# Kernel optimization log

Hardware: AMD Instinct MI355X
Metric: run time of the kernel (lower is better)

Reference implementation:

```python
import jax, jax.numpy as jnp
from jax import lax
import numpy as np

K = 1024      # kernel_size
S = 256       # stride
CUT = 513     # kernel_size//2 + 1
TC = 2 * CUT  # transform_channels = 1026
CH = 8        # combine_hidden
B = 32
TIME = 262144


def setup_inputs() -> dict:
    key = jax.random.key(0)
    ks = jax.random.split(key, 12)
    x = jax.random.normal(ks[0], (B, 1, TIME), dtype=jnp.float32)
    conv1_w = jax.random.normal(ks[1], (TC, 1, K), dtype=jnp.float32) * 0.02
    in_gamma = 1.0 + 0.1 * jax.random.normal(ks[2], (TC,), dtype=jnp.float32)
    comb1_w = jax.random.normal(ks[3], (CH, 2), dtype=jnp.float32) * 0.5
    comb1_b = jax.random.normal(ks[4], (CH,), dtype=jnp.float32) * 0.1
    comb2_w = jax.random.normal(ks[5], (1, CH), dtype=jnp.float32) * 0.5
    comb2_b = jax.random.normal(ks[6], (1,), dtype=jnp.float32) * 0.1
    lin_w = jax.random.normal(ks[7], (CUT, CUT), dtype=jnp.float32) * 0.04
    lin_b = jax.random.normal(ks[8], (CUT,), dtype=jnp.float32) * 0.02
    fc_gamma = 1.0 + 0.1 * jax.random.normal(ks[9], (CUT,), dtype=jnp.float32)
    convT_w = jax.random.normal(ks[10], (TC, 2, K), dtype=jnp.float32) * 0.02  # torch ConvTranspose1d (Cin, Cout, K)
    return {"x": x, "conv1_w": conv1_w, "in_gamma": in_gamma,
            "comb1_w": comb1_w, "comb1_b": comb1_b,
            "comb2_w": comb2_w, "comb2_b": comb2_b,
            "lin_w": lin_w, "lin_b": lin_b, "fc_gamma": fc_gamma,
            "convT_w": convT_w}


def reference(x, conv1_w, in_gamma, comb1_w, comb1_b, comb2_w, comb2_b,
              lin_w, lin_b, fc_gamma, convT_w):
    time = x.shape[2]
    # conv1: Conv1d(1, TC, K, stride=S, padding=K), no bias
    t = lax.conv_general_dilated(x, conv1_w, window_strides=(S,),
                                 padding=[(K, K)],
                                 dimension_numbers=("NCH", "OIH", "NCH"))
    # ConvScaler1d (per-channel scale) + tanh activation
    t = jnp.tanh(t * in_gamma[None, :, None])  # (B, TC, F)
    real_x, imag_x = t[:, :CUT, :], t[:, CUT:, :]
    spec = jnp.stack([real_x, imag_x], axis=1)  # (B, 2, CUT, F)
    # combine1/combine2: 1x1 Conv2d + relu
    h = jax.nn.relu(jnp.einsum("bcxf,oc->boxf", spec, comb1_w)
                    + comb1_b[None, :, None, None])
    h = jax.nn.relu(jnp.einsum("bcxf,oc->boxf", h, comb2_w)
                    + comb2_b[None, :, None, None])[:, 0]  # (B, CUT, F)
    # FC over frequency axis per (batch, frame)
    hh = h.transpose(0, 2, 1)  # (B, F, CUT)
    hh = (hh @ lin_w.T + lin_b) * fc_gamma  # BitwiseLinear + Scaler
    mask = (jnp.tanh(hh) + 1.0) * 0.5       # output_transform -> [0,1]
    mask = mask.transpose(0, 2, 1)          # (B, CUT, F)
    mask = jnp.concatenate([mask, mask], axis=1)  # (B, TC, F)
    t = t * mask
    # conv1_transpose: ConvTranspose1d(TC, 2, K, stride=S), no bias
    wt = jnp.flip(convT_w.transpose(1, 0, 2), axis=2)  # (2, TC, K) flipped
    y = lax.conv_general_dilated(t, wt, window_strides=(1,),
                                 padding=[(K - 1, K - 1)],
                                 lhs_dilation=(S,),
                                 dimension_numbers=("NCH", "OIH", "NCH"))
    y = y[:, :, K:time + K]  # (B, 2, time)
    return jax.nn.softmax(y, axis=1)
```

## Files before the change

kernel.cpp:

```cpp
#include <hip/hip_runtime.h>
#include <cstddef>
#include <cstdint>

#define TIME_N 262144
#define BATCH  32
#define KW     1024
#define ST     256
#define CUTN   513
#define TCN    1026
#define FN     1029
#define FPAD   1152
#define CPAD   1152
#define XLEN   (FPAD * ST + KW)
#define XBLK   (XLEN / 256)

#define MROWS  (BATCH * FN)
#define MP     33024
#define KPH    544
#define NPH    640
#define TBP    1032
#define FLATB  (FN * TBP)
#define KPC    4128

#define PB_XPAD  (XBLK * BATCH)
#define PB_WBF   (PB_XPAD + CPAD)
#define PB_WLIN  (PB_WBF + NPH)
#define PB_TOTAL (PB_WLIN + KPC)

typedef __bf16 bf16x8 __attribute__((ext_vector_type(8)));
typedef float floatx4 __attribute__((ext_vector_type(4)));

__device__ __forceinline__ unsigned short f2bf(float f) {
    union { float f; unsigned u; } v; v.f = f;
    unsigned r = (v.u + 0x7fffu + ((v.u >> 16) & 1u)) >> 16;
    return (unsigned short)r;
}
__device__ __forceinline__ float bf2f(unsigned short s) {
    union { unsigned u; float f; } v; v.u = ((unsigned)s) << 16;
    return v.f;
}
__device__ __forceinline__ int permch(int n) {
    return (n & 1) ? (CUTN + (n >> 1)) : (n >> 1);
}

__device__ __forceinline__ void load_lds16(const void* g, void* l) {
    __builtin_amdgcn_global_load_lds(
        (const __attribute__((address_space(1))) void*)g,
        (__attribute__((address_space(3))) void*)l, 16, 0, 0);
}

__global__ __launch_bounds__(256) void k_prep(
    const float* __restrict__ x, const float* __restrict__ c1w,
    const float* __restrict__ lw, const float* __restrict__ wct,
    unsigned short* __restrict__ xb, unsigned short* __restrict__ wbf,
    unsigned short* __restrict__ wlb, unsigned short* __restrict__ wdb)
{
    const int bid = blockIdx.x;
    if (bid < PB_XPAD) {
        const int b = bid / XBLK;
        const int p = (bid - b * XBLK) * 256 + threadIdx.x;
        const int g = p - KW;
        float v = (g >= 0 && g < TIME_N) ? x[(size_t)b * TIME_N + g] : 0.0f;
        xb[(size_t)b * XLEN + p] = f2bf(v);
    } else if (bid < PB_WBF) {
        const int n = bid - PB_XPAD;
        const int ch = (n < TCN) ? permch(n) : 0;
        for (int k = threadIdx.x; k < KW; k += 256) {
            float v = (n < TCN) ? c1w[(size_t)ch * KW + k] : 0.0f;
            wbf[(size_t)n * KW + k] = f2bf(v);
        }
    } else if (bid < PB_WLIN) {
        const int n = bid - PB_WBF;
        for (int k = threadIdx.x; k < KPH; k += 256) {
            float v = (n < CUTN && k < CUTN) ? lw[(size_t)n * CUTN + k] : 0.0f;
            wlb[(size_t)n * KPH + k] = f2bf(v);
        }
    } else {
        const int k = bid - PB_WLIN;
        const int r = threadIdx.x;
        const int j = k / TBP;
        const int n = k - j * TBP;
        float v = 0.0f;
        if (n < TCN) {
            const int ch = permch(n);
            const int widx = (3 - j) * 256 + r;
            v = wct[(size_t)(2 * ch) * KW + widx] -
                wct[(size_t)(2 * ch + 1) * KW + widx];
        }
        wdb[(size_t)r * KPC + k] = f2bf(v);
    }
}

__global__ __launch_bounds__(256) void k_conv1m(
    const unsigned short* __restrict__ xb, const unsigned short* __restrict__ wb,
    const float* __restrict__ gamma,
    const float* __restrict__ c1w, const float* __restrict__ c1b,
    const float* __restrict__ c2w, const float* __restrict__ c2b,
    unsigned short* __restrict__ tb2, unsigned short* __restrict__ h)
{
    __shared__ __align__(16) unsigned short As[128 * 32];
    __shared__ __align__(16) unsigned short Bs[128 * 32];

    const int b = blockIdx.x, fb = blockIdx.y, cb = blockIdx.z;
    const int f0 = fb * 128, c0 = cb * 128;
    const int tid = threadIdx.x;

    const int s0 = tid, s1 = tid + 256;
    const int ar0 = s0 >> 2, aq0 = s0 & 3;
    const int ar1 = s1 >> 2, aq1 = s1 & 3;
    const unsigned short* xrow = xb + (size_t)b * XLEN;
    const unsigned short* ga0 = xrow + (size_t)(f0 + ar0) * ST + aq0 * 8;
    const unsigned short* ga1 = xrow + (size_t)(f0 + ar1) * ST + aq1 * 8;
    const unsigned short* gb0 = wb + (size_t)(c0 + ar0) * KW + aq0 * 8;
    const unsigned short* gb1 = wb + (size_t)(c0 + ar1) * KW + aq1 * 8;
    unsigned short* la0 = &As[s0 * 8];
    unsigned short* la1 = &As[s1 * 8];
    unsigned short* lb0 = &Bs[s0 * 8];
    unsigned short* lb1 = &Bs[s1 * 8];

    const int wave = tid >> 6, lane = tid & 63;
    const int lm = lane & 15, lq = lane >> 4;
    const int mw = (wave & 1) * 64, nw = (wave >> 1) * 64;
    const unsigned short* Ap = &As[(mw + lm) * 32 + lq * 8];
    const unsigned short* Bp = &Bs[(nw + lm) * 32 + lq * 8];

    floatx4 acc[4][4];
#pragma unroll
    for (int i = 0; i < 4; ++i)
#pragma unroll
        for (int j = 0; j < 4; ++j) acc[i][j] = (floatx4)0.0f;

    for (int ks = 0; ks < KW / 32; ++ks) {
        load_lds16(ga0, la0);
        load_lds16(ga1, la1);
        load_lds16(gb0, lb0);
        load_lds16(gb1, lb1);
        ga0 += 32; ga1 += 32; gb0 += 32; gb1 += 32;
        __syncthreads();

        bf16x8 afr[4], bfr[4];
#pragma unroll
        for (int mt = 0; mt < 4; ++mt) afr[mt] = *(const bf16x8*)(Ap + mt * 16 * 32);
#pragma unroll
        for (int nt = 0; nt < 4; ++nt) bfr[nt] = *(const bf16x8*)(Bp + nt * 16 * 32);
#pragma unroll
        for (int mt = 0; mt < 4; ++mt)
#pragma unroll
            for (int nt = 0; nt < 4; ++nt)
                acc[mt][nt] = __builtin_amdgcn_mfma_f32_16x16x32_bf16(
                    afr[mt], bfr[nt], acc[mt][nt], 0, 0, 0);
        __syncthreads();
    }

    float w1[16], b1[8], w2[8];
#pragma unroll
    for (int o = 0; o < 8; ++o) {
        w1[2 * o]     = c1w[2 * o];
        w1[2 * o + 1] = c1w[2 * o + 1];
        b1[o] = c1b[o];
        w2[o] = c2w[o];
    }
    const float b2v = c2b[0];

    unsigned short* tbb = tb2 + (size_t)b * FLATB;
    const bool evenlane = ((lane & 1) == 0);
#pragma unroll
    for (int nt = 0; nt < 4; ++nt) {
        const int n = c0 + nw + nt * 16 + lm;
        const bool valid_c = (n < TCN);
        const float gv = valid_c ? gamma[permch(n)] : 0.0f;
        const int nbase = n & ~1;
        const int ybase = n >> 1;
        const bool store_c = (nbase < TBP);
#pragma unroll
        for (int mt = 0; mt < 4; ++mt) {
#pragma unroll
            for (int rp = 0; rp < 2; ++rp) {
                const int ra = rp * 2;
                const int fa = f0 + mw + mt * 16 + lq * 4 + ra;
                const float ua = acc[mt][nt][ra] * gv;
                const float ub = acc[mt][nt][ra + 1] * gv;
                const float ta  = 2.0f / (1.0f + __expf(-2.0f * ua)) - 1.0f;
                const float tbv = 2.0f / (1.0f + __expf(-2.0f * ub)) - 1.0f;
                const float sa = __shfl_xor(ta, 1);
                const float sb = __shfl_xor(tbv, 1);
                const int  fme = evenlane ? fa : (fa + 1);
                const float re = evenlane ? ta : sb;
                const float im = evenlane ? sa : tbv;
                if (fme < FN) {
                    if (store_c) {
                        const unsigned pr = (unsigned)f2bf(re) |
                                            ((unsigned)f2bf(im) << 16);
                        *(unsigned*)&tbb[(size_t)fme * TBP + nbase] = pr;
                    }
                    if (valid_c) {
                        float a2 = b2v;
#pragma unroll
                        for (int o = 0; o < 8; ++o) {
                            const float a1 = fmaxf(
                                re * w1[2 * o] + im * w1[2 * o + 1] + b1[o], 0.0f);
                            a2 += a1 * w2[o];
                        }
                        h[((size_t)b * FN + fme) * KPH + ybase] =
                            f2bf(fmaxf(a2, 0.0f));
                    }
                }
            }
        }
    }
}

__global__ __launch_bounds__(256) void k_maskm(
    const unsigned short* __restrict__ h, const unsigned short* __restrict__ wlb,
    const float* __restrict__ linb, const float* __restrict__ fcg,
    unsigned* __restrict__ tbu)
{
    __shared__ __align__(16) unsigned short As[128 * 32];
    __shared__ __align__(16) unsigned short Bs[128 * 32];

    const int m0 = blockIdx.x * 128, n0 = blockIdx.y * 128;
    const int tid = threadIdx.x;

    const int s0 = tid, s1 = tid + 256;
    const int ar0 = s0 >> 2, aq0 = s0 & 3;
    const int ar1 = s1 >> 2, aq1 = s1 & 3;
    const unsigned short* ga0 = h + (size_t)(m0 + ar0) * KPH + aq0 * 8;
    const unsigned short* ga1 = h + (size_t)(m0 + ar1) * KPH + aq1 * 8;
    const unsigned short* gb0 = wlb + (size_t)(n0 + ar0) * KPH + aq0 * 8;
    const unsigned short* gb1 = wlb + (size_t)(n0 + ar1) * KPH + aq1 * 8;
    unsigned short* la0 = &As[s0 * 8];
    unsigned short* la1 = &As[s1 * 8];
    unsigned short* lb0 = &Bs[s0 * 8];
    unsigned short* lb1 = &Bs[s1 * 8];

    const int wave = tid >> 6, lane = tid & 63;
    const int lm = lane & 15, lq = lane >> 4;
    const int mw = (wave & 1) * 64, nw = (wave >> 1) * 64;
    const unsigned short* Ap = &As[(mw + lm) * 32 + lq * 8];
    const unsigned short* Bp = &Bs[(nw + lm) * 32 + lq * 8];

    floatx4 acc[4][4];
#pragma unroll
    for (int i = 0; i < 4; ++i)
#pragma unroll
        for (int j = 0; j < 4; ++j) acc[i][j] = (floatx4)0.0f;

    for (int ks = 0; ks < KPH / 32; ++ks) {
        load_lds16(ga0, la0);
        load_lds16(ga1, la1);
        load_lds16(gb0, lb0);
        load_lds16(gb1, lb1);
        ga0 += 32; ga1 += 32; gb0 += 32; gb1 += 32;
        __syncthreads();

        bf16x8 afr[4], bfr[4];
#pragma unroll
        for (int mt = 0; mt < 4; ++mt) afr[mt] = *(const bf16x8*)(Ap + mt * 16 * 32);
#pragma unroll
        for (int nt = 0; nt < 4; ++nt) bfr[nt] = *(const bf16x8*)(Bp + nt * 16 * 32);
#pragma unroll
        for (int mt = 0; mt < 4; ++mt)
#pragma unroll
            for (int nt = 0; nt < 4; ++nt)
                acc[mt][nt] = __builtin_amdgcn_mfma_f32_16x16x32_bf16(
                    afr[mt], bfr[nt], acc[mt][nt], 0, 0, 0);
        __syncthreads();
    }

#pragma unroll
    for (int nt = 0; nt < 4; ++nt) {
        const int y = n0 + nw + nt * 16 + lm;
        if (y < CUTN) {
            const float lb = linb[y];
            const float gv = fcg[y];
#pragma unroll
            for (int mt = 0; mt < 4; ++mt) {
#pragma unroll
                for (int r = 0; r < 4; ++r) {
                    const int m = m0 + mw + mt * 16 + lq * 4 + r;
                    if (m < MROWS) {
                        const float v = (acc[mt][nt][r] + lb) * gv;
                        const float msk = 1.0f / (1.0f + __expf(-2.0f * v));
                        unsigned* p = tbu + (size_t)m * (TBP / 2) + y;
                        const unsigned u = *p;
                        const float re = bf2f((unsigned short)(u & 0xffffu)) * msk;
                        const float im = bf2f((unsigned short)(u >> 16)) * msk;
                        *p = (unsigned)f2bf(re) | ((unsigned)f2bf(im) << 16);
                    }
                }
            }
        }
    }
}

__global__ __launch_bounds__(256) void k_convtm(
    const unsigned short* __restrict__ tb2, const unsigned short* __restrict__ wdb,
    float* __restrict__ out)
{
    __shared__ __align__(16) unsigned short As[128 * 32];
    __shared__ __align__(16) unsigned short Bs[128 * 32];

    const int m0 = blockIdx.x * 128, n0 = blockIdx.y * 128;
    const int b   = m0 >> 10;
    const int ml0 = m0 & 1023;
    const int tid = threadIdx.x;

    const int s0 = tid, s1 = tid + 256;
    const int ar0 = s0 >> 2, aq0 = s0 & 3;
    const int ar1 = s1 >> 2, aq1 = s1 & 3;
    const unsigned short* tbb = tb2 + (size_t)b * FLATB;
    const unsigned short* ga0 = tbb + (size_t)(ml0 + ar0 + 1) * TBP + aq0 * 8;
    const unsigned short* ga1 = tbb + (size_t)(ml0 + ar1 + 1) * TBP + aq1 * 8;
    const unsigned short* gb0 = wdb + (size_t)(n0 + ar0) * KPC + aq0 * 8;
    const unsigned short* gb1 = wdb + (size_t)(n0 + ar1) * KPC + aq1 * 8;
    unsigned short* la0 = &As[s0 * 8];
    unsigned short* la1 = &As[s1 * 8];
    unsigned short* lb0 = &Bs[s0 * 8];
    unsigned short* lb1 = &Bs[s1 * 8];

    const int wave = tid >> 6, lane = tid & 63;
    const int lm = lane & 15, lq = lane >> 4;
    const int mw = (wave & 1) * 64, nw = (wave >> 1) * 64;
    const unsigned short* Ap = &As[(mw + lm) * 32 + lq * 8];
    const unsigned short* Bp = &Bs[(nw + lm) * 32 + lq * 8];

    floatx4 acc[4][4];
#pragma unroll
    for (int i = 0; i < 4; ++i)
#pragma unroll
        for (int j = 0; j < 4; ++j) acc[i][j] = (floatx4)0.0f;

    for (int ks = 0; ks < KPC / 32; ++ks) {
        load_lds16(ga0, la0);
        load_lds16(ga1, la1);
        load_lds16(gb0, lb0);
        load_lds16(gb1, lb1);
        ga0 += 32; ga1 += 32; gb0 += 32; gb1 += 32;
        __syncthreads();

        bf16x8 afr[4], bfr[4];
#pragma unroll
        for (int mt = 0; mt < 4; ++mt) afr[mt] = *(const bf16x8*)(Ap + mt * 16 * 32);
#pragma unroll
        for (int nt = 0; nt < 4; ++nt) bfr[nt] = *(const bf16x8*)(Bp + nt * 16 * 32);
#pragma unroll
        for (int mt = 0; mt < 4; ++mt)
#pragma unroll
            for (int nt = 0; nt < 4; ++nt)
                acc[mt][nt] = __builtin_amdgcn_mfma_f32_16x16x32_bf16(
                    afr[mt], bfr[nt], acc[mt][nt], 0, 0, 0);
        __syncthreads();
    }

    float* ob = out + (size_t)b * 2 * TIME_N;
#pragma unroll
    for (int nt = 0; nt < 4; ++nt) {
        const int n = n0 + nw + nt * 16 + lm;
#pragma unroll
        for (int mt = 0; mt < 4; ++mt) {
#pragma unroll
            for (int r = 0; r < 4; ++r) {
                const int m = ml0 + mw + mt * 16 + lq * 4 + r;
                const float d = acc[mt][nt][r];
                const float p0 = 1.0f / (1.0f + __expf(-d));
                const int tau = m * 256 + n;
                ob[tau]          = p0;
                ob[TIME_N + tau] = 1.0f - p0;
            }
        }
    }
}

extern "C" void kernel_launch(void* const* d_in, const int* in_sizes, int n_in,
                              void* d_out, int out_size, void* d_ws, size_t ws_size,
                              hipStream_t stream)
{
    const float* x    = (const float*)d_in[0];
    const float* c1w  = (const float*)d_in[1];
    const float* ing  = (const float*)d_in[2];
    const float* cb1w = (const float*)d_in[3];
    const float* cb1b = (const float*)d_in[4];
    const float* cb2w = (const float*)d_in[5];
    const float* cb2b = (const float*)d_in[6];
    const float* linw = (const float*)d_in[7];
    const float* linb = (const float*)d_in[8];
    const float* fcg  = (const float*)d_in[9];
    const float* ctw  = (const float*)d_in[10];
    float* out = (float*)d_out;

    unsigned short* tb2 = (unsigned short*)d_ws;
    unsigned short* h   = tb2 + (size_t)BATCH * FLATB;
    unsigned short* wlb = h + (size_t)MP * KPH;
    unsigned short* xb  = wlb + (size_t)NPH * KPH;
    unsigned short* wbf = xb + (size_t)BATCH * XLEN;
    unsigned short* wdb = wbf + (size_t)CPAD * KW;

    hipLaunchKernelGGL(k_prep, dim3(PB_TOTAL), dim3(256), 0, stream,
                       x, c1w, linw, ctw, xb, wbf, wlb, wdb);
    hipLaunchKernelGGL(k_conv1m, dim3(BATCH, 9, 9), dim3(256), 0, stream,
                       xb, wbf, ing, cb1w, cb1b, cb2w, cb2b, tb2, h);
    hipLaunchKernelGGL(k_maskm, dim3(MP / 128, NPH / 128), dim3(256), 0, stream,
                       h, wlb, linb, fcg, (unsigned*)tb2);
    hipLaunchKernelGGL(k_convtm, dim3(256, 2), dim3(256), 0, stream,
                       tb2, wdb, out);
}
```

Measured before the change: 512.0 us.

## Retile conv1 GEMM to 256x256x64 with double-buffered swizzled LDS

Rewrites the conv1 im2col GEMM kernel to use 256x256 tiles with BK=64 and 512 threads. Batch and frame are flattened into one M dimension. LDS is double-buffered in 64KB halves with an XOR swizzle, so the next tile loads while the MFMAs run, and s_setprio and barriers interleave fragment loads with compute. The goal is to cut per-tile global/LDS traffic and barrier stalls and raise MFMA utilisation. The cost is 128KB of dynamic LDS, high register pressure, and partial tiles in N (1026 of 1280 columns used), which wastes some work.

```diff
diff --git a/kernel.cpp b/kernel.cpp
--- a/kernel.cpp
+++ b/kernel.cpp
@@ -26,6 +26,14 @@
 #define PB_WBF   (PB_XPAD + CPAD)
 #define PB_WLIN  (PB_WBF + NPH)
 #define PB_TOTAL (PB_WLIN + KPC)
+
+#define C1_BM   256
+#define C1_BN   256
+#define C1_BK   64
+#define C1_NT   (KW / C1_BK)
+#define C1_MB   129
+#define C1_NB   5
+#define C1_BUF  65536
 
 typedef __bf16 bf16x8 __attribute__((ext_vector_type(8)));
 typedef float floatx4 __attribute__((ext_vector_type(4)));
@@ -91,118 +99,209 @@
     }
 }
 
-__global__ __launch_bounds__(256) void k_conv1m(
+__global__ __launch_bounds__(512, 2) void k_conv1m(
     const unsigned short* __restrict__ xb, const unsigned short* __restrict__ wb,
     const float* __restrict__ gamma,
     const float* __restrict__ c1w, const float* __restrict__ c1b,
     const float* __restrict__ c2w, const float* __restrict__ c2b,
     unsigned short* __restrict__ tb2, unsigned short* __restrict__ h)
 {
-    __shared__ __align__(16) unsigned short As[128 * 32];
-    __shared__ __align__(16) unsigned short Bs[128 * 32];
-
-    const int b = blockIdx.x, fb = blockIdx.y, cb = blockIdx.z;
-    const int f0 = fb * 128, c0 = cb * 128;
+    extern __shared__ char lds[];
+    const int m0 = blockIdx.x * C1_BM;
+    const int n0 = blockIdx.y * C1_BN;
     const int tid = threadIdx.x;
-
-    const int s0 = tid, s1 = tid + 256;
-    const int ar0 = s0 >> 2, aq0 = s0 & 3;
-    const int ar1 = s1 >> 2, aq1 = s1 & 3;
-    const unsigned short* xrow = xb + (size_t)b * XLEN;
-    const unsigned short* ga0 = xrow + (size_t)(f0 + ar0) * ST + aq0 * 8;
-    const unsigned short* ga1 = xrow + (size_t)(f0 + ar1) * ST + aq1 * 8;
-    const unsigned short* gb0 = wb + (size_t)(c0 + ar0) * KW + aq0 * 8;
-    const unsigned short* gb1 = wb + (size_t)(c0 + ar1) * KW + aq1 * 8;
-    unsigned short* la0 = &As[s0 * 8];
-    unsigned short* la1 = &As[s1 * 8];
-    unsigned short* lb0 = &Bs[s0 * 8];
-    unsigned short* lb1 = &Bs[s1 * 8];
-
-    const int wave = tid >> 6, lane = tid & 63;
+    const int wv = tid >> 6, lane = tid & 63;
     const int lm = lane & 15, lq = lane >> 4;
-    const int mw = (wave & 1) * 64, nw = (wave >> 1) * 64;
-    const unsigned short* Ap = &As[(mw + lm) * 32 + lq * 8];
-    const unsigned short* Bp = &Bs[(nw + lm) * 32 + lq * 8];
-
-    floatx4 acc[4][4];
-#pragma unroll
-    for (int i = 0; i < 4; ++i)
+    const int wr = wv >> 2, wc = wv & 3;
+
+    const unsigned short* src[8];
+    int ldsq[8];
+#pragma unroll
+    for (int i = 0; i < 8; ++i) {
+        const int c = wv * 8 + i;
+        const int q = c * 1024 + lane * 16;
+        ldsq[i] = q;
+        const int sec = q >> 14;
+        const int p = q & 16383;
+        const int row = p >> 7;
+        const int cb = (p & 127) ^ ((row & 7) << 4);
+        const int e = cb >> 1;
+        if (sec < 2) {
+            int m = m0 + sec * 128 + row;
+            if (m >= MROWS) m = 0;
+            const int b = m / FN;
+            const int f = m - b * FN;
+            src[i] = xb + (size_t)b * XLEN + (size_t)f * ST + e;
+        } else {
+            int n = n0 + (sec - 2) * 128 + row;
+            if (n > CPAD - 1) n = CPAD - 1;
+            src[i] = wb + (size_t)n * KW + e;
+        }
+    }
+
+    const int swz = (lm & 7) << 4;
+    int abo[2], bbo[2];
+#pragma unroll
+    for (int ks = 0; ks < 2; ++ks) {
+        abo[ks] = wr * 16384 + lm * 128 + ((ks * 64 + lq * 16) ^ swz);
+        bbo[ks] = 32768 + (wc >> 1) * 16384 + ((wc & 1) * 64 + lm) * 128
+                  + ((ks * 64 + lq * 16) ^ swz);
+    }
+
+    floatx4 acc[8][4];
+#pragma unroll
+    for (int i = 0; i < 8; ++i)
 #pragma unroll
         for (int j = 0; j < 4; ++j) acc[i][j] = (floatx4)0.0f;
 
-    for (int ks = 0; ks < KW / 32; ++ks) {
-        load_lds16(ga0, la0);
-        load_lds16(ga1, la1);
-        load_lds16(gb0, lb0);
-        load_lds16(gb1, lb1);
-        ga0 += 32; ga1 += 32; gb0 += 32; gb1 += 32;
+#pragma unroll
+    for (int i = 0; i < 8; ++i) {
+        load_lds16(src[i], lds + ldsq[i]);
+        src[i] += C1_BK;
+    }
+    __syncthreads();
+
+    for (int t = 0; t < C1_NT; ++t) {
+        char* cur = lds + (t & 1) * C1_BUF;
+        char* nxt = lds + ((t + 1) & 1) * C1_BUF;
+        bf16x8 af[4][2], bf[2][2];
+
+#pragma unroll
+        for (int mt = 0; mt < 4; ++mt)
+#pragma unroll
+            for (int ks = 0; ks < 2; ++ks)
+                af[mt][ks] = *(const bf16x8*)(cur + abo[ks] + mt * 2048);
+#pragma unroll
+        for (int nt = 0; nt < 2; ++nt)
+#pragma unroll
+            for (int ks = 0; ks < 2; ++ks)
+                bf[nt][ks] = *(const bf16x8*)(cur + bbo[ks] + nt * 2048);
+        if (t + 1 < C1_NT) {
+#pragma unroll
+            for (int i = 0; i < 8; ++i) {
+                load_lds16(src[i], nxt + ldsq[i]);
+                src[i] += C1_BK;
+            }
+        }
+        __builtin_amdgcn_s_barrier();
+        __builtin_amdgcn_s_setprio(1);
+#pragma unroll
+        for (int mt = 0; mt < 4; ++mt)
+#pragma unroll
+            for (int nt = 0; nt < 2; ++nt)
+#pragma unroll
+                for (int ks = 0; ks < 2; ++ks)
+                    acc[mt][nt] = __builtin_amdgcn_mfma_f32_16x16x32_bf16(
+                        af[mt][ks], bf[nt][ks], acc[mt][nt], 0, 0, 0);
+        __builtin_amdgcn_s_setprio(0);
+        __builtin_amdgcn_s_barrier();
+
+#pragma unroll
+        for (int nt = 0; nt < 2; ++nt)
+#pragma unroll
+            for (int ks = 0; ks < 2; ++ks)
+                bf[nt][ks] = *(const bf16x8*)(cur + bbo[ks] + (2 + nt) * 2048);
+        __builtin_amdgcn_s_barrier();
+        __builtin_amdgcn_s_setprio(1);
+#pragma unroll
+        for (int mt = 0; mt < 4; ++mt)
+#pragma unroll
+            for (int nt = 0; nt < 2; ++nt)
+#pragma unroll
+                for (int ks = 0; ks < 2; ++ks)
+                    acc[mt][2 + nt] = __builtin_amdgcn_mfma_f32_16x16x32_bf16(
+                        af[mt][ks], bf[nt][ks], acc[mt][2 + nt], 0, 0, 0);
+        __builtin_amdgcn_s_setprio(0);
+        __builtin_amdgcn_s_barrier();
+
+#pragma unroll
+        for (int mt = 0; mt < 4; ++mt)
+#pragma unroll
+            for (int ks = 0; ks < 2; ++ks)
+                af[mt][ks] = *(const bf16x8*)(cur + abo[ks] + (4 + mt) * 2048);
+        __builtin_amdgcn_s_barrier();
+        __builtin_amdgcn_s_setprio(1);
+#pragma unroll
+        for (int mt = 0; mt < 4; ++mt)
+#pragma unroll
+            for (int nt = 0; nt < 2; ++nt)
+#pragma unroll
+                for (int ks = 0; ks < 2; ++ks)
+                    acc[4 + mt][2 + nt] = __builtin_amdgcn_mfma_f32_16x16x32_bf16(
+                        af[mt][ks], bf[nt][ks], acc[4 + mt][2 + nt], 0, 0, 0);
+        __builtin_amdgcn_s_setprio(0);
+        __builtin_amdgcn_s_barrier();
+
+#pragma unroll
+        for (int nt = 0; nt < 2; ++nt)
+#pragma unroll
+            for (int ks = 0; ks < 2; ++ks)
+                bf[nt][ks] = *(const bf16x8*)(cur + bbo[ks] + nt * 2048);
+        __builtin_amdgcn_s_barrier();
+        __builtin_amdgcn_s_setprio(1);
+#pragma unroll
+        for (int mt = 0; mt < 4; ++mt)
+#pragma unroll
+            for (int nt = 0; nt < 2; ++nt)
+#pragma unroll
+                for (int ks = 0; ks < 2; ++ks)
+                    acc[4 + mt][nt] = __builtin_amdgcn_mfma_f32_16x16x32_bf16(
+                        af[mt][ks], bf[nt][ks], acc[4 + mt][nt], 0, 0, 0);
+        __builtin_amdgcn_s_setprio(0);
         __syncthreads();
-
-        bf16x8 afr[4], bfr[4];
-#pragma unroll
-        for (int mt = 0; mt < 4; ++mt) afr[mt] = *(const bf16x8*)(Ap + mt * 16 * 32);
-#pragma unroll
-        for (int nt = 0; nt < 4; ++nt) bfr[nt] = *(const bf16x8*)(Bp + nt * 16 * 32);
-#pragma unroll
-        for (int mt = 0; mt < 4; ++mt)
-#pragma unroll
-            for (int nt = 0; nt < 4; ++nt)
-                acc[mt][nt] = __builtin_amdgcn_mfma_f32_16x16x32_bf16(
-                    afr[mt], bfr[nt], acc[mt][nt], 0, 0, 0);
-        __syncthreads();
-    }
-
-    float w1[16], b1[8], w2[8];
+    }
+
+    float w1[16], b1v[8], w2[8];
 #pragma unroll
     for (int o = 0; o < 8; ++o) {
         w1[2 * o]     = c1w[2 * o];
         w1[2 * o + 1] = c1w[2 * o + 1];
-        b1[o] = c1b[o];
+        b1v[o] = c1b[o];
         w2[o] = c2w[o];
     }
     const float b2v = c2b[0];
-
-    unsigned short* tbb = tb2 + (size_t)b * FLATB;
     const bool evenlane = ((lane & 1) == 0);
-#pragma unroll
-    for (int nt = 0; nt < 4; ++nt) {
-        const int n = c0 + nw + nt * 16 + lm;
+
+#pragma unroll
+    for (int ni = 0; ni < 4; ++ni) {
+        const int n = n0 + wc * 64 + ni * 16 + lm;
         const bool valid_c = (n < TCN);
         const float gv = valid_c ? gamma[permch(n)] : 0.0f;
         const int nbase = n & ~1;
         const int ybase = n >> 1;
         const bool store_c = (nbase < TBP);
 #pragma unroll
-        for (int mt = 0; mt < 4; ++mt) {
+        for (int mi = 0; mi < 8; ++mi) {
 #pragma unroll
             for (int rp = 0; rp < 2; ++rp) {
                 const int ra = rp * 2;
-                const int fa = f0 + mw + mt * 16 + lq * 4 + ra;
-                const float ua = acc[mt][nt][ra] * gv;
-                const float ub = acc[mt][nt][ra + 1] * gv;
+                const int mrow = m0 + wr * 128 + mi * 16 + lq * 4 + ra;
+                const float ua = acc[mi][ni][ra] * gv;
+                const float ub = acc[mi][ni][ra + 1] * gv;
                 const float ta  = 2.0f / (1.0f + __expf(-2.0f * ua)) - 1.0f;
                 const float tbv = 2.0f / (1.0f + __expf(-2.0f * ub)) - 1.0f;
                 const float sa = __shfl_xor(ta, 1);
                 const float sb = __shfl_xor(tbv, 1);
-                const int  fme = evenlane ? fa : (fa + 1);
+                const int  fme = evenlane ? mrow : (mrow + 1);
                 const float re = evenlane ? ta : sb;
                 const float im = evenlane ? sa : tbv;
-                if (fme < FN) {
+                if (fme < MROWS) {
+                    const int b = fme / FN;
+                    const int f = fme - b * FN;
                     if (store_c) {
                         const unsigned pr = (unsigned)f2bf(re) |
                                             ((unsigned)f2bf(im) << 16);
-                        *(unsigned*)&tbb[(size_t)fme * TBP + nbase] = pr;
+                        *(unsigned*)&tb2[(size_t)b * FLATB + (size_t)f * TBP + nbase] = pr;
                     }
                     if (valid_c) {
                         float a2 = b2v;
 #pragma unroll
                         for (int o = 0; o < 8; ++o) {
                             const float a1 = fmaxf(
-                                re * w1[2 * o] + im * w1[2 * o + 1] + b1[o], 0.0f);
+                                re * w1[2 * o] + im * w1[2 * o + 1] + b1v[o], 0.0f);
                             a2 += a1 * w2[o];
                         }
-                        h[((size_t)b * FN + fme) * KPH + ybase] =
-                            f2bf(fmaxf(a2, 0.0f));
+                        h[(size_t)fme * KPH + ybase] = f2bf(fmaxf(a2, 0.0f));
                     }
                 }
             }
@@ -397,7 +496,7 @@
 
     hipLaunchKernelGGL(k_prep, dim3(PB_TOTAL), dim3(256), 0, stream,
                        x, c1w, linw, ctw, xb, wbf, wlb, wdb);
-    hipLaunchKernelGGL(k_conv1m, dim3(BATCH, 9, 9), dim3(256), 0, stream,
+    hipLaunchKernelGGL(k_conv1m, dim3(C1_MB, C1_NB), dim3(512), 2 * C1_BUF, stream,
                        xb, wbf, ing, cb1w, cb1b, cb2w, cb2b, tb2, h);
     hipLaunchKernelGGL(k_maskm, dim3(MP / 128, NPH / 128), dim3(256), 0, stream,
                        h, wlb, linb, fcg, (unsigned*)tb2);
```

Measured after the change: 629.4 us. 22.9% more time.

## Double GEMM K-tile to 64 and XOR-swizzle LDS layout in conv kernels

Applied to the files above, without the earlier changes.

Both MFMA GEMM kernels (conv1 and transposed conv) now stage 64-wide K slices per iteration instead of 32, which halves the number of barrier pairs per K loop. The LDS tiles use an XOR swizzle on 16-byte chunks keyed by row, so fragment reads avoid bank conflicts. TBP and KPC padding grow to multiples of 64 so the K loop divides evenly. In exchange, LDS per block doubles and register pressure rises with two fragments per tile, which could reduce occupancy.

```diff
diff --git a/kernel.cpp b/kernel.cpp
--- a/kernel.cpp
+++ b/kernel.cpp
@@ -18,9 +18,9 @@
 #define MP     33024
 #define KPH    544
 #define NPH    640
-#define TBP    1032
+#define TBP    1040
 #define FLATB  (FN * TBP)
-#define KPC    4128
+#define KPC    4160
 
 #define PB_XPAD  (XBLK * BATCH)
 #define PB_WBF   (PB_XPAD + CPAD)
@@ -98,31 +98,38 @@
     const float* __restrict__ c2w, const float* __restrict__ c2b,
     unsigned short* __restrict__ tb2, unsigned short* __restrict__ h)
 {
-    __shared__ __align__(16) unsigned short As[128 * 32];
-    __shared__ __align__(16) unsigned short Bs[128 * 32];
+    __shared__ __align__(16) unsigned short As[128 * 64];
+    __shared__ __align__(16) unsigned short Bs[128 * 64];
 
     const int b = blockIdx.x, fb = blockIdx.y, cb = blockIdx.z;
     const int f0 = fb * 128, c0 = cb * 128;
     const int tid = threadIdx.x;
 
-    const int s0 = tid, s1 = tid + 256;
-    const int ar0 = s0 >> 2, aq0 = s0 & 3;
-    const int ar1 = s1 >> 2, aq1 = s1 & 3;
     const unsigned short* xrow = xb + (size_t)b * XLEN;
-    const unsigned short* ga0 = xrow + (size_t)(f0 + ar0) * ST + aq0 * 8;
-    const unsigned short* ga1 = xrow + (size_t)(f0 + ar1) * ST + aq1 * 8;
-    const unsigned short* gb0 = wb + (size_t)(c0 + ar0) * KW + aq0 * 8;
-    const unsigned short* gb1 = wb + (size_t)(c0 + ar1) * KW + aq1 * 8;
-    unsigned short* la0 = &As[s0 * 8];
-    unsigned short* la1 = &As[s1 * 8];
-    unsigned short* lb0 = &Bs[s0 * 8];
-    unsigned short* lb1 = &Bs[s1 * 8];
+    const unsigned short* ga[4];
+    const unsigned short* gb[4];
+    int qa[4];
+#pragma unroll
+    for (int i = 0; i < 4; ++i) {
+        const int c = i * 256 + tid;
+        const int row = c >> 3;
+        const int colb = (c & 7) * 16;
+        const int es = (colb ^ ((row & 7) << 4)) >> 1;
+        qa[i] = c * 16;
+        ga[i] = xrow + (size_t)(f0 + row) * ST + es;
+        gb[i] = wb + (size_t)(c0 + row) * KW + es;
+    }
 
     const int wave = tid >> 6, lane = tid & 63;
     const int lm = lane & 15, lq = lane >> 4;
     const int mw = (wave & 1) * 64, nw = (wave >> 1) * 64;
-    const unsigned short* Ap = &As[(mw + lm) * 32 + lq * 8];
-    const unsigned short* Bp = &Bs[(nw + lm) * 32 + lq * 8];
+    const int swz = (lm & 7) << 4;
+    int abo[2], bbo[2];
+#pragma unroll
+    for (int ks = 0; ks < 2; ++ks) {
+        abo[ks] = (mw + lm) * 128 + ((ks * 64 + lq * 16) ^ swz);
+        bbo[ks] = (nw + lm) * 128 + ((ks * 64 + lq * 16) ^ swz);
+    }
 
     floatx4 acc[4][4];
 #pragma unroll
@@ -130,25 +137,37 @@
 #pragma unroll
         for (int j = 0; j < 4; ++j) acc[i][j] = (floatx4)0.0f;
 
-    for (int ks = 0; ks < KW / 32; ++ks) {
-        load_lds16(ga0, la0);
-        load_lds16(ga1, la1);
-        load_lds16(gb0, lb0);
-        load_lds16(gb1, lb1);
-        ga0 += 32; ga1 += 32; gb0 += 32; gb1 += 32;
-        __syncthreads();
-
-        bf16x8 afr[4], bfr[4];
-#pragma unroll
-        for (int mt = 0; mt < 4; ++mt) afr[mt] = *(const bf16x8*)(Ap + mt * 16 * 32);
-#pragma unroll
-        for (int nt = 0; nt < 4; ++nt) bfr[nt] = *(const bf16x8*)(Bp + nt * 16 * 32);
+    const char* Ab = (const char*)As;
+    const char* Bb = (const char*)Bs;
+
+    for (int t = 0; t < KW / 64; ++t) {
+#pragma unroll
+        for (int i = 0; i < 4; ++i) {
+            load_lds16(ga[i], (char*)As + qa[i]);
+            load_lds16(gb[i], (char*)Bs + qa[i]);
+            ga[i] += 64; gb[i] += 64;
+        }
+        __syncthreads();
+
+        bf16x8 afr[4][2], bfr[4][2];
 #pragma unroll
         for (int mt = 0; mt < 4; ++mt)
 #pragma unroll
+            for (int ks = 0; ks < 2; ++ks)
+                afr[mt][ks] = *(const bf16x8*)(Ab + abo[ks] + mt * 2048);
+#pragma unroll
+        for (int nt = 0; nt < 4; ++nt)
+#pragma unroll
+            for (int ks = 0; ks < 2; ++ks)
+                bfr[nt][ks] = *(const bf16x8*)(Bb + bbo[ks] + nt * 2048);
+#pragma unroll
+        for (int mt = 0; mt < 4; ++mt)
+#pragma unroll
             for (int nt = 0; nt < 4; ++nt)
-                acc[mt][nt] = __builtin_amdgcn_mfma_f32_16x16x32_bf16(
-                    afr[mt], bfr[nt], acc[mt][nt], 0, 0, 0);
+#pragma unroll
+                for (int ks = 0; ks < 2; ++ks)
+                    acc[mt][nt] = __builtin_amdgcn_mfma_f32_16x16x32_bf16(
+                        afr[mt][ks], bfr[nt][ks], acc[mt][nt], 0, 0, 0);
         __syncthreads();
     }
 
@@ -297,32 +316,39 @@
     const unsigned short* __restrict__ tb2, const unsigned short* __restrict__ wdb,
     float* __restrict__ out)
 {
-    __shared__ __align__(16) unsigned short As[128 * 32];
-    __shared__ __align__(16) unsigned short Bs[128 * 32];
+    __shared__ __align__(16) unsigned short As[128 * 64];
+    __shared__ __align__(16) unsigned short Bs[128 * 64];
 
     const int m0 = blockIdx.x * 128, n0 = blockIdx.y * 128;
     const int b   = m0 >> 10;
     const int ml0 = m0 & 1023;
     const int tid = threadIdx.x;
 
-    const int s0 = tid, s1 = tid + 256;
-    const int ar0 = s0 >> 2, aq0 = s0 & 3;
-    const int ar1 = s1 >> 2, aq1 = s1 & 3;
     const unsigned short* tbb = tb2 + (size_t)b * FLATB;
-    const unsigned short* ga0 = tbb + (size_t)(ml0 + ar0 + 1) * TBP + aq0 * 8;
-    const unsigned short* ga1 = tbb + (size_t)(ml0 + ar1 + 1) * TBP + aq1 * 8;
-    const unsigned short* gb0 = wdb + (size_t)(n0 + ar0) * KPC + aq0 * 8;
-    const unsigned short* gb1 = wdb + (size_t)(n0 + ar1) * KPC + aq1 * 8;
-    unsigned short* la0 = &As[s0 * 8];
-    unsigned short* la1 = &As[s1 * 8];
-    unsigned short* lb0 = &Bs[s0 * 8];
-    unsigned short* lb1 = &Bs[s1 * 8];
+    const unsigned short* ga[4];
+    const unsigned short* gb[4];
+    int qa[4];
+#pragma unroll
+    for (int i = 0; i < 4; ++i) {
+        const int c = i * 256 + tid;
+        const int row = c >> 3;
+        const int colb = (c & 7) * 16;
+        const int es = (colb ^ ((row & 7) << 4)) >> 1;
+        qa[i] = c * 16;
+        ga[i] = tbb + (size_t)(ml0 + row + 1) * TBP + es;
+        gb[i] = wdb + (size_t)(n0 + row) * KPC + es;
+    }
 
     const int wave = tid >> 6, lane = tid & 63;
     const int lm = lane & 15, lq = lane >> 4;
     const int mw = (wave & 1) * 64, nw = (wave >> 1) * 64;
-    const unsigned short* Ap = &As[(mw + lm) * 32 + lq * 8];
-    const unsigned short* Bp = &Bs[(nw + lm) * 32 + lq * 8];
+    const int swz = (lm & 7) << 4;
+    int abo[2], bbo[2];
+#pragma unroll
+    for (int ks = 0; ks < 2; ++ks) {
+        abo[ks] = (mw + lm) * 128 + ((ks * 64 + lq * 16) ^ swz);
+        bbo[ks] = (nw + lm) * 128 + ((ks * 64 + lq * 16) ^ swz);
+    }
 
     floatx4 acc[4][4];
 #pragma unroll
@@ -330,25 +356,37 @@
 #pragma unroll
         for (int j = 0; j < 4; ++j) acc[i][j] = (floatx4)0.0f;
 
-    for (int ks = 0; ks < KPC / 32; ++ks) {
-        load_lds16(ga0, la0);
-        load_lds16(ga1, la1);
-        load_lds16(gb0, lb0);
-        load_lds16(gb1, lb1);
-        ga0 += 32; ga1 += 32; gb0 += 32; gb1 += 32;
-        __syncthreads();
-
-        bf16x8 afr[4], bfr[4];
-#pragma unroll
-        for (int mt = 0; mt < 4; ++mt) afr[mt] = *(const bf16x8*)(Ap + mt * 16 * 32);
-#pragma unroll
-        for (int nt = 0; nt < 4; ++nt) bfr[nt] = *(const bf16x8*)(Bp + nt * 16 * 32);
+    const char* Ab = (const char*)As;
+    const char* Bb = (const char*)Bs;
+
+    for (int t = 0; t < KPC / 64; ++t) {
+#pragma unroll
+        for (int i = 0; i < 4; ++i) {
+            load_lds16(ga[i], (char*)As + qa[i]);
+            load_lds16(gb[i], (char*)Bs + qa[i]);
+            ga[i] += 64; gb[i] += 64;
+        }
+        __syncthreads();
+
+        bf16x8 afr[4][2], bfr[4][2];
 #pragma unroll
         for (int mt = 0; mt < 4; ++mt)
 #pragma unroll
+            for (int ks = 0; ks < 2; ++ks)
+                afr[mt][ks] = *(const bf16x8*)(Ab + abo[ks] + mt * 2048);
+#pragma unroll
+        for (int nt = 0; nt < 4; ++nt)
+#pragma unroll
+            for (int ks = 0; ks < 2; ++ks)
+                bfr[nt][ks] = *(const bf16x8*)(Bb + bbo[ks] + nt * 2048);
+#pragma unroll
+        for (int mt = 0; mt < 4; ++mt)
+#pragma unroll
             for (int nt = 0; nt < 4; ++nt)
-                acc[mt][nt] = __builtin_amdgcn_mfma_f32_16x16x32_bf16(
-                    afr[mt], bfr[nt], acc[mt][nt], 0, 0, 0);
+#pragma unroll
+                for (int ks = 0; ks < 2; ++ks)
+                    acc[mt][nt] = __builtin_amdgcn_mfma_f32_16x16x32_bf16(
+                        afr[mt][ks], bfr[nt][ks], acc[mt][nt], 0, 0, 0);
         __syncthreads();
     }
 
```

Result: faster. 471.3 us (-7.9%).
